# Kernel tuning notes

Measured on AMD Instinct MI355X. Metric: run time of the kernel, lower is better.

The kernel has to match this reference:

```python
import jax, jax.numpy as jnp
import numpy as np

TOKEN_DIM = 32
NQ, LQ = 16, 128   # query (label-description) batch and length
ND, LD = 128, 128  # doc batch and length
VOCAB = 1000


def setup_inputs() -> dict:
    key = jax.random.key(0)
    k1, k2, k3, k4 = jax.random.split(key, 4)
    return {
        "doc_reps": jax.random.normal(k1, (ND, LD, TOKEN_DIM), dtype=jnp.float32),
        "qry_reps": jax.random.normal(k2, (NQ, LQ, TOKEN_DIM), dtype=jnp.float32),
        "qry_attention_mask": jnp.ones((NQ, LQ), dtype=jnp.float32),
        "doc_input_ids": jax.random.randint(k3, (ND, LD), 0, VOCAB).astype(jnp.int64),
        "qry_input_ids": jax.random.randint(k4, (NQ, LQ), 0, VOCAB).astype(jnp.int64),
    }


def reference(doc_reps, qry_reps, qry_attention_mask, doc_input_ids, qry_input_ids):
    # exact-match mask: [NQ, LQ, ND, LD]
    exact_match = qry_input_ids[:, :, None, None] == doc_input_ids[None, None, :, :]
    # full cartesian token similarity: [NQ, LQ, ND, LD]
    scores_no_masking = jnp.einsum("qid,njd->qinj", qry_reps, doc_reps)
    # COIL: zero out non-exact-match pairs, MaxSim over doc tokens -> [NQ, LQ, ND]
    scores = jnp.where(exact_match, scores_no_masking, 0.0).max(axis=3)
    # masked sum over query tokens, skipping position 0 ([CLS]) -> [NQ, ND]
    tok_scores = (scores * qry_attention_mask[:, :, None])[:, 1:].sum(axis=1)
    return tok_scores
```

## Files before the change

### kernel.cpp

```cpp
#include <hip/hip_runtime.h>

#define TOKEN_DIM 32
#define NQ 16
#define LQ 128
#define ND 128
#define LD 128

__global__ __launch_bounds__(128) void coil_maxsim_kernel(
    const float* __restrict__ doc_reps,
    const float* __restrict__ qry_reps,
    const float* __restrict__ qry_mask,
    const int*   __restrict__ doc_ids,
    const int*   __restrict__ qry_ids,
    float*       __restrict__ out)
{
    __shared__ int   s_ids[LD];
    __shared__ float s_red[2];

    const int bid = blockIdx.x;
    const int q   = bid >> 7;
    const int n   = bid & 127;
    const int tid = threadIdx.x;

    s_ids[tid] = doc_ids[n * LD + tid];
    const int qid = qry_ids[q * LQ + tid];
    __syncthreads();

    unsigned m[4];
    const int4* ids4 = (const int4*)s_ids;
    #pragma unroll
    for (int w = 0; w < 4; ++w) {
        unsigned mm = 0;
        #pragma unroll
        for (int p = 0; p < 8; ++p) {
            int4 a = ids4[w * 8 + p];
            mm |= (unsigned)(a.x == qid) << (4 * p + 0);
            mm |= (unsigned)(a.y == qid) << (4 * p + 1);
            mm |= (unsigned)(a.z == qid) << (4 * p + 2);
            mm |= (unsigned)(a.w == qid) << (4 * p + 3);
        }
        m[w] = mm;
    }
    const int nmatch = __popc(m[0]) + __popc(m[1]) + __popc(m[2]) + __popc(m[3]);

    float4 qr[8];
    if (nmatch != 0) {
        const float4* qv = (const float4*)(qry_reps + (size_t)(q * LQ + tid) * TOKEN_DIM);
        #pragma unroll
        for (int k = 0; k < 8; ++k) qr[k] = qv[k];
    }

    const float4* dbase = (const float4*)(doc_reps + (size_t)n * LD * TOKEN_DIM);
    float best = -INFINITY;
    #pragma unroll
    for (int w = 0; w < 4; ++w) {
        unsigned mm = m[w];
        while (__any(mm != 0)) {
            if (mm) {
                const int j = (w << 5) + __ffs(mm) - 1;
                mm &= mm - 1;
                const float4* dv = dbase + j * (TOKEN_DIM / 4);
                float acc = 0.f;
                #pragma unroll
                for (int k = 0; k < 8; ++k) {
                    float4 d = dv[k];
                    acc += qr[k].x * d.x + qr[k].y * d.y + qr[k].z * d.z + qr[k].w * d.w;
                }
                best = fmaxf(best, acc);
            }
        }
    }
    if (nmatch < LD) best = fmaxf(best, 0.0f);

    float partial = (tid >= 1) ? best * qry_mask[q * LQ + tid] : 0.0f;
    #pragma unroll
    for (int off = 32; off > 0; off >>= 1)
        partial += __shfl_down(partial, off);
    if ((tid & 63) == 0) s_red[tid >> 6] = partial;
    __syncthreads();
    if (tid == 0) out[q * ND + n] = s_red[0] + s_red[1];
}

extern "C" void kernel_launch(void* const* d_in, const int* in_sizes, int n_in,
                              void* d_out, int out_size, void* d_ws, size_t ws_size,
                              hipStream_t stream) {
    const float* doc_reps = (const float*)d_in[0];
    const float* qry_reps = (const float*)d_in[1];
    const float* qry_mask = (const float*)d_in[2];
    const int*   doc_ids  = (const int*)d_in[3];
    const int*   qry_ids  = (const int*)d_in[4];
    float* out = (float*)d_out;

    coil_maxsim_kernel<<<dim3(NQ * ND), dim3(128), 0, stream>>>(
        doc_reps, qry_reps, qry_mask, doc_ids, qry_ids, out);
}
```

Measured before the change: 13.06 us.

## Process eight queries per block, reusing doc ids across queries

Each block now handles one doc and eight queries: 256 threads, each covering four queries for a single query token position. The doc ids are loaded once straight from global memory into registers and compared against four query ids, replacing the shared-memory staging and its barrier. The grid shrinks from 2048 blocks to 256, which cuts launch and per-block overhead but lowers parallelism on a large-CU GPU and raises register use from the 4x4 mask array.

New measurement: 16.35 us. 1.25x slower.

```diff
diff --git a/kernel.cpp b/kernel.cpp
--- a/kernel.cpp
+++ b/kernel.cpp
@@ -6,7 +6,7 @@
 #define ND 128
 #define LD 128
 
-__global__ __launch_bounds__(128) void coil_maxsim_kernel(
+__global__ __launch_bounds__(256) void coil_maxsim_kernel(
     const float* __restrict__ doc_reps,
     const float* __restrict__ qry_reps,
     const float* __restrict__ qry_mask,
@@ -14,71 +14,97 @@
     const int*   __restrict__ qry_ids,
     float*       __restrict__ out)
 {
-    __shared__ int   s_ids[LD];
-    __shared__ float s_red[2];
+    __shared__ float s_red[8][2];
 
-    const int bid = blockIdx.x;
-    const int q   = bid >> 7;
-    const int n   = bid & 127;
-    const int tid = threadIdx.x;
+    const int bid  = blockIdx.x;
+    const int n    = bid & (ND - 1);
+    const int qh   = bid >> 7;
+    const int tid  = threadIdx.x;
+    const int i    = tid & (LQ - 1);
+    const int qsub = tid >> 7;
 
-    s_ids[tid] = doc_ids[n * LD + tid];
-    const int qid = qry_ids[q * LQ + tid];
-    __syncthreads();
+    int   qid[4];
+    float msk[4];
+    #pragma unroll
+    for (int k = 0; k < 4; ++k) {
+        const int q = qh * 8 + qsub * 4 + k;
+        qid[k] = qry_ids[q * LQ + i];
+        msk[k] = qry_mask[q * LQ + i];
+    }
 
-    unsigned m[4];
-    const int4* ids4 = (const int4*)s_ids;
+    unsigned m[4][4];
+    const int4* dip = (const int4*)(doc_ids + n * LD);
     #pragma unroll
     for (int w = 0; w < 4; ++w) {
-        unsigned mm = 0;
+        int4 c[8];
         #pragma unroll
-        for (int p = 0; p < 8; ++p) {
-            int4 a = ids4[w * 8 + p];
-            mm |= (unsigned)(a.x == qid) << (4 * p + 0);
-            mm |= (unsigned)(a.y == qid) << (4 * p + 1);
-            mm |= (unsigned)(a.z == qid) << (4 * p + 2);
-            mm |= (unsigned)(a.w == qid) << (4 * p + 3);
+        for (int p = 0; p < 8; ++p) c[p] = dip[w * 8 + p];
+        #pragma unroll
+        for (int k = 0; k < 4; ++k) {
+            unsigned mm = 0;
+            #pragma unroll
+            for (int p = 0; p < 8; ++p) {
+                mm |= (unsigned)(c[p].x == qid[k]) << (4 * p + 0);
+                mm |= (unsigned)(c[p].y == qid[k]) << (4 * p + 1);
+                mm |= (unsigned)(c[p].z == qid[k]) << (4 * p + 2);
+                mm |= (unsigned)(c[p].w == qid[k]) << (4 * p + 3);
+            }
+            m[k][w] = mm;
         }
-        m[w] = mm;
-    }
-    const int nmatch = __popc(m[0]) + __popc(m[1]) + __popc(m[2]) + __popc(m[3]);
-
-    float4 qr[8];
-    if (nmatch != 0) {
-        const float4* qv = (const float4*)(qry_reps + (size_t)(q * LQ + tid) * TOKEN_DIM);
-        #pragma unroll
-        for (int k = 0; k < 8; ++k) qr[k] = qv[k];
     }
 
     const float4* dbase = (const float4*)(doc_reps + (size_t)n * LD * TOKEN_DIM);
-    float best = -INFINITY;
+
     #pragma unroll
-    for (int w = 0; w < 4; ++w) {
-        unsigned mm = m[w];
-        while (__any(mm != 0)) {
-            if (mm) {
-                const int j = (w << 5) + __ffs(mm) - 1;
-                mm &= mm - 1;
-                const float4* dv = dbase + j * (TOKEN_DIM / 4);
-                float acc = 0.f;
-                #pragma unroll
-                for (int k = 0; k < 8; ++k) {
-                    float4 d = dv[k];
-                    acc += qr[k].x * d.x + qr[k].y * d.y + qr[k].z * d.z + qr[k].w * d.w;
+    for (int k = 0; k < 4; ++k) {
+        unsigned long long M0 = (unsigned long long)m[k][0] |
+                                ((unsigned long long)m[k][1] << 32);
+        unsigned long long M1 = (unsigned long long)m[k][2] |
+                                ((unsigned long long)m[k][3] << 32);
+        const int nmatch = __popcll(M0) + __popcll(M1);
+
+        float4 qr[8];
+        if (nmatch != 0) {
+            const int q = qh * 8 + qsub * 4 + k;
+            const float4* qv = (const float4*)(qry_reps +
+                               (size_t)(q * LQ + i) * TOKEN_DIM);
+            #pragma unroll
+            for (int kk = 0; kk < 8; ++kk) qr[kk] = qv[kk];
+        }
+
+        float best = -INFINITY;
+        #pragma unroll
+        for (int h = 0; h < 2; ++h) {
+            unsigned long long mm = h ? M1 : M0;
+            const int jb = h * 64;
+            while (__any(mm != 0)) {
+                if (mm) {
+                    const int j = jb + __ffsll(mm) - 1;
+                    mm &= mm - 1;
+                    const float4* dv = dbase + j * (TOKEN_DIM / 4);
+                    float acc = 0.f;
+                    #pragma unroll
+                    for (int kk = 0; kk < 8; ++kk) {
+                        float4 d = dv[kk];
+                        acc += qr[kk].x * d.x + qr[kk].y * d.y +
+                               qr[kk].z * d.z + qr[kk].w * d.w;
+                    }
+                    best = fmaxf(best, acc);
                 }
-                best = fmaxf(best, acc);
             }
         }
+        if (nmatch < LD) best = fmaxf(best, 0.0f);
+
+        float p = (i >= 1) ? best * msk[k] : 0.0f;
+        #pragma unroll
+        for (int off = 32; off > 0; off >>= 1)
+            p += __shfl_down(p, off);
+        if ((tid & 63) == 0) s_red[qsub * 4 + k][(tid >> 6) & 1] = p;
     }
-    if (nmatch < LD) best = fmaxf(best, 0.0f);
 
-    float partial = (tid >= 1) ? best * qry_mask[q * LQ + tid] : 0.0f;
-    #pragma unroll
-    for (int off = 32; off > 0; off >>= 1)
-        partial += __shfl_down(partial, off);
-    if ((tid & 63) == 0) s_red[tid >> 6] = partial;
     __syncthreads();
-    if (tid == 0) out[q * ND + n] = s_red[0] + s_red[1];
+    if (tid < 8)
+        out[(qh * 8 + tid) * ND + n] = s_red[tid][0] + s_red[tid][1];
 }
 
 extern "C" void kernel_launch(void* const* d_in, const int* in_sizes, int n_in,
@@ -91,6 +117,6 @@
     const int*   qry_ids  = (const int*)d_in[4];
     float* out = (float*)d_out;
 
-    coil_maxsim_kernel<<<dim3(NQ * ND), dim3(128), 0, stream>>>(
+    coil_maxsim_kernel<<<dim3(ND * (NQ / 8)), dim3(256), 0, stream>>>(
         doc_reps, qry_reps, qry_mask, doc_ids, qry_ids, out);
 }
```
